# Optimization experiments

Hardware: AMD Instinct MI355X
Metric: run time of the kernel (lower is better)

Reference implementation:

```python
import jax, jax.numpy as jnp
import numpy as np

EMBED_DIM = 4096
NUM_Q_HEADS = 32
NUM_KV_HEADS = 8
HEAD_DIM = EMBED_DIM // NUM_Q_HEADS  # 128
GROUP = NUM_Q_HEADS // NUM_KV_HEADS  # 4
KV_SEQ_LEN = 1024
BATCH = 2
SEQ = 1024
THETA = 10000.0


def _rope(x, positions):
    # x: (B, T, H, D) with interleaved real/imag pairs along D (torch view_as_complex layout)
    half = x.shape[-1] // 2
    inv_freq = 1.0 / (THETA ** (jnp.arange(half, dtype=jnp.float32) / half))
    ang = positions[:, None].astype(jnp.float32) * inv_freq[None, :]  # (T, half)
    cos = jnp.cos(ang)[None, :, None, :].astype(x.dtype)
    sin = jnp.sin(ang)[None, :, None, :].astype(x.dtype)
    xr = x.reshape(*x.shape[:-1], half, 2)
    x0, x1 = xr[..., 0], xr[..., 1]
    o0 = x0 * cos - x1 * sin
    o1 = x0 * sin + x1 * cos
    return jnp.stack([o0, o1], axis=-1).reshape(x.shape)


def setup_inputs() -> dict:
    key = jax.random.key(0)
    ks = jax.random.split(key, 5)
    s_in = 1.0 / np.sqrt(EMBED_DIM)
    return {
        "x": jax.random.normal(ks[0], (BATCH, SEQ, EMBED_DIM), dtype=jnp.float32),
        "Wq": jax.random.normal(ks[1], (EMBED_DIM, EMBED_DIM), dtype=jnp.float32) * s_in,
        "Wk": jax.random.normal(ks[2], (NUM_KV_HEADS * HEAD_DIM, EMBED_DIM), dtype=jnp.float32) * s_in,
        "Wv": jax.random.normal(ks[3], (NUM_KV_HEADS * HEAD_DIM, EMBED_DIM), dtype=jnp.float32) * s_in,
        "Wo": jax.random.normal(ks[4], (EMBED_DIM, EMBED_DIM), dtype=jnp.float32) * s_in,
        "cache_k": jnp.zeros((BATCH, 2 * KV_SEQ_LEN, NUM_KV_HEADS, HEAD_DIM), dtype=jnp.float32),
        "cache_v": jnp.zeros((BATCH, 2 * KV_SEQ_LEN, NUM_KV_HEADS, HEAD_DIM), dtype=jnp.float32),
        "start_pos": 0,
    }


def reference(x, Wq, Wk, Wv, Wo, cache_k, cache_v, start_pos):
    B, T, C = x.shape
    end_pos = start_pos + T
    scale = 1.0 / np.sqrt(HEAD_DIM)

    q = (x @ Wq.T).reshape(B, T, NUM_Q_HEADS, HEAD_DIM)
    k = (x @ Wk.T).reshape(B, T, NUM_KV_HEADS, HEAD_DIM)
    v = (x @ Wv.T).reshape(B, T, NUM_KV_HEADS, HEAD_DIM)

    pos = start_pos + jnp.arange(T)
    q = _rope(q, pos)
    k = _rope(k, pos)

    # KV cache append (writes are detached in the original)
    cache_k = cache_k.at[:, start_pos:end_pos].set(jax.lax.stop_gradient(k))
    cache_v = cache_v.at[:, start_pos:end_pos].set(jax.lax.stop_gradient(v))
    k_full = cache_k[:, :end_pos]  # (B, S, Hkv, D)
    v_full = cache_v[:, :end_pos]

    # GQA without materializing repeated KV heads:
    # q head h attends kv head h // GROUP (matches repeat_interleave layout)
    q5 = q.transpose(0, 2, 1, 3).reshape(B, NUM_KV_HEADS, GROUP, T, HEAD_DIM)
    kh = k_full.transpose(0, 2, 1, 3)  # (B, Hkv, S, D)
    vh = v_full.transpose(0, 2, 1, 3)

    scores = jnp.einsum('bhgtd,bhsd->bhgts', q5, kh) * scale  # (B,Hkv,G,T,S)
    visible = jnp.arange(end_pos)[None, :] <= (start_pos + jnp.arange(T))[:, None]  # (T,S)
    scores = jnp.where(visible[None, None, None], scores, jnp.finfo(scores.dtype).min)
    probs = jax.nn.softmax(scores, axis=-1)
    ctx = jnp.einsum('bhgts,bhsd->bhgtd', probs, vh)

    out = ctx.reshape(B, NUM_Q_HEADS, T, HEAD_DIM).transpose(0, 2, 1, 3).reshape(B, T, C)
    return out @ Wo.T
```

## Files before the change

kernel.cpp:

```cpp
#include <hip/hip_runtime.h>
#include <stdint.h>

typedef unsigned short u16;
typedef __attribute__((ext_vector_type(8))) short short8x;
typedef __attribute__((ext_vector_type(4))) float floatx4;

#define TOKENS 2048
#define EMBED  4096
#define QKVN   6144
#define T_SEQ  1024
#define SMAX   2048
#define NQH    32
#define NKVH   8
#define HD     128

static __device__ __forceinline__ u16 f2b(float f) {
    union { float f; uint32_t u; } v; v.f = f;
    uint32_t r = v.u + 0x7fffu + ((v.u >> 16) & 1u);
    return (u16)(r >> 16);
}
static __device__ __forceinline__ float b2f(u16 h) {
    union { uint32_t u; float f; } v; v.u = ((uint32_t)h) << 16; return v.f;
}

static __device__ __forceinline__ void gload_lds16(const u16* g, u16* l) {
    __builtin_amdgcn_global_load_lds(
        (const __attribute__((address_space(1))) uint32_t*)g,
        (__attribute__((address_space(3))) uint32_t*)l, 16, 0, 0);
}

#define CSEG0 2097152
#define CSEG1 6291456
#define CSEG2 7340032
#define CSEG3 8388608
#define CSEG4 12582912
__global__ void convert_all_kernel(const float* __restrict__ x,  const float* __restrict__ Wq,
                                   const float* __restrict__ Wk, const float* __restrict__ Wv,
                                   const float* __restrict__ Wo,
                                   u16* __restrict__ xb, u16* __restrict__ wqkv,
                                   u16* __restrict__ wob) {
    int i = blockIdx.x * blockDim.x + threadIdx.x;
    if (i >= CSEG4) return;
    const float4* src; uint2* dst; int off;
    if (i < CSEG0)      { src = (const float4*)x;  dst = (uint2*)xb;   off = i; }
    else if (i < CSEG1) { src = (const float4*)Wq; dst = (uint2*)wqkv; off = i - CSEG0; }
    else if (i < CSEG2) { src = (const float4*)Wk; dst = (uint2*)wqkv + 4194304; off = i - CSEG1; }
    else if (i < CSEG3) { src = (const float4*)Wv; dst = (uint2*)wqkv + 5242880; off = i - CSEG2; }
    else                { src = (const float4*)Wo; dst = (uint2*)wob;  off = i - CSEG3; }
    float4 f = src[off];
    union { u16 h[4]; uint2 v; } o;
    o.h[0] = f2b(f.x); o.h[1] = f2b(f.y); o.h[2] = f2b(f.z); o.h[3] = f2b(f.w);
    dst[off] = o.v;
}

#define FENCE asm volatile("" ::: "memory")
#define WAITZ asm volatile("s_waitcnt vmcnt(0)" ::: "memory")
#define NOSTG ((void)0)
#define NOW   ((void)0)

#define HBA(BUF, H) (lds + (BUF) * 28672 + (H) * 8192)
#define HBB(BUF)    (lds + (BUF) * 28672 + 16384)
#define STGA(BUF, H, KT) do { \
    gload_lds16(gA[H][0] + (size_t)(KT) * 64, HBA(BUF, H) + dOffW); \
    gload_lds16(gA[H][1] + (size_t)(KT) * 64, HBA(BUF, H) + 4096 + dOffW); \
} while (0)
#define STGB(BUF, KT) do { \
    _Pragma("unroll") \
    for (int _L = 0; _L < 3; _L++) \
        gload_lds16(gBv[_L] + (size_t)(KT) * 64, HBB(BUF) + _L * 4096 + dOffW); \
} while (0)
#define STGALL(BUF, KT) do { STGA(BUF, 0, KT); STGA(BUF, 1, KT); STGB(BUF, KT); } while (0)
#define PH1(CBUF, STAGES, ENDW) do { \
    const u16* _pa0 = HBA(CBUF, 0); \
    const u16* _pa1 = HBA(CBUF, 1); \
    const u16* _pb  = HBB(CBUF); \
    short8x af0[4][2], af1[4][2], bf[3][2]; \
    _Pragma("unroll") \
    for (int _mi = 0; _mi < 4; _mi++) { \
        af0[_mi][0] = *(const short8x*)(_pa0 + offA[_mi][0]); \
        af0[_mi][1] = *(const short8x*)(_pa0 + offA[_mi][1]); } \
    _Pragma("unroll") \
    for (int _nj = 0; _nj < 3; _nj++) { \
        bf[_nj][0] = *(const short8x*)(_pb + offB[_nj][0]); \
        bf[_nj][1] = *(const short8x*)(_pb + offB[_nj][1]); } \
    STAGES; \
    __builtin_amdgcn_sched_barrier(0); \
    _Pragma("unroll") \
    for (int _mi = 0; _mi < 4; _mi++) { \
        af1[_mi][0] = *(const short8x*)(_pa1 + offA[_mi][0]); \
        af1[_mi][1] = *(const short8x*)(_pa1 + offA[_mi][1]); } \
    __builtin_amdgcn_s_setprio(1); \
    _Pragma("unroll") \
    for (int _kk = 0; _kk < 2; _kk++) \
        _Pragma("unroll") \
        for (int _mi = 0; _mi < 4; _mi++) \
            _Pragma("unroll") \
            for (int _nj = 0; _nj < 3; _nj++) \
                acc[0][_mi][_nj] = __builtin_amdgcn_mfma_f32_16x16x32_bf16( \
                    af0[_mi][_kk], bf[_nj][_kk], acc[0][_mi][_nj], 0, 0, 0); \
    _Pragma("unroll") \
    for (int _kk = 0; _kk < 2; _kk++) \
        _Pragma("unroll") \
        for (int _mi = 0; _mi < 4; _mi++) \
            _Pragma("unroll") \
            for (int _nj = 0; _nj < 3; _nj++) \
                acc[1][_mi][_nj] = __builtin_amdgcn_mfma_f32_16x16x32_bf16( \
                    af1[_mi][_kk], bf[_nj][_kk], acc[1][_mi][_nj], 0, 0, 0); \
    __builtin_amdgcn_s_setprio(0); \
    ENDW; \
    FENCE; __builtin_amdgcn_s_barrier(); FENCE; \
} while (0)

__global__ __launch_bounds__(512, 1) void gemm256_kernel(
    const u16* __restrict__ A, const u16* __restrict__ Bw,
    u16* __restrict__ Cv, int N, int K) {
    extern __shared__ __align__(16) u16 lds[];
    const int tid = threadIdx.x;
    const int lane = tid & 63, w = tid >> 6;
    const int quad = lane >> 4, lc = lane & 15;
    const int wm = w >> 2, wn = w & 3;
    const int Mbase = blockIdx.y * 256, Nbase = blockIdx.x * 192;

    const int r8 = lane >> 3;
    const int sl = (lane & 7) ^ r8;
    const int srow = w * 8 + r8;
    const u16* gA[2][2];
    const u16* gBv[3];
#pragma unroll
    for (int H = 0; H < 2; H++)
#pragma unroll
        for (int L = 0; L < 2; L++)
            gA[H][L] = A + (size_t)(Mbase + H * 128 + L * 64 + srow) * K + sl * 8;
#pragma unroll
    for (int L = 0; L < 3; L++)
        gBv[L] = Bw + (size_t)(Nbase + L * 64 + srow) * K + sl * 8;
    const int dOffW = w * 512;

    int offA[4][2], offB[3][2];
    const int xsw = lc & 7;
#pragma unroll
    for (int mi = 0; mi < 4; mi++)
#pragma unroll
        for (int kk = 0; kk < 2; kk++)
            offA[mi][kk] = (wm * 64 + mi * 16 + lc) * 64 + (((kk * 4 + quad) ^ xsw) * 8);
#pragma unroll
    for (int nj = 0; nj < 3; nj++)
#pragma unroll
        for (int kk = 0; kk < 2; kk++)
            offB[nj][kk] = (wn * 48 + nj * 16 + lc) * 64 + (((kk * 4 + quad) ^ xsw) * 8);

    floatx4 acc[2][4][3] = {};

    STGALL(0, 0);
    WAITZ;
    FENCE; __builtin_amdgcn_s_barrier(); FENCE;

    const int NT = K >> 6;
    for (int t = 0; t < NT - 2; t += 2) {
        PH1(0, STGALL(1, t + 1), WAITZ);
        PH1(1, STGALL(0, t + 2), WAITZ);
    }
    PH1(0, STGALL(1, NT - 1), WAITZ);
    PH1(1, NOSTG, NOW);

#pragma unroll
    for (int AH = 0; AH < 2; AH++)
#pragma unroll
        for (int mi = 0; mi < 4; mi++) {
            const int row0 = Mbase + AH * 128 + wm * 64 + mi * 16 + quad * 4;
#pragma unroll
            for (int nj = 0; nj < 3; nj++) {
                const int col = Nbase + wn * 48 + nj * 16 + lc;
#pragma unroll
                for (int r = 0; r < 4; r++)
                    Cv[(size_t)(row0 + r) * N + col] = f2b(acc[AH][mi][nj][r]);
            }
        }
}
#undef HBA
#undef HBB
#undef STGA
#undef STGB
#undef STGALL
#undef PH1

#define HA2(BUF, H) (lds + (BUF) * 24576 + (H) * 4096)
#define HBB2(BUF)   (lds + (BUF) * 24576 + 8192)
#define STGA2(BUF, H, KT) gload_lds16(gA2[H] + (size_t)(KT) * 64, HA2(BUF, H) + dOffW)
#define STGB2(BUF, KT) do { \
    _Pragma("unroll") \
    for (int _L = 0; _L < 4; _L++) \
        gload_lds16(gB2[_L] + (size_t)(KT) * 64, HBB2(BUF) + _L * 4096 + dOffW); \
} while (0)
#define STGALL2(BUF, KT) do { STGA2(BUF, 0, KT); STGA2(BUF, 1, KT); STGB2(BUF, KT); } while (0)
#define PH2(CBUF, STAGES, ENDW) do { \
    const u16* _pa0 = HA2(CBUF, 0); \
    const u16* _pa1 = HA2(CBUF, 1); \
    const u16* _pb  = HBB2(CBUF); \
    short8x af0[2][2], af1[2][2], bf2[4][2]; \
    _Pragma("unroll") \
    for (int _mi = 0; _mi < 2; _mi++) { \
        af0[_mi][0] = *(const short8x*)(_pa0 + offA2[_mi][0]); \
        af0[_mi][1] = *(const short8x*)(_pa0 + offA2[_mi][1]); } \
    _Pragma("unroll") \
    for (int _nj = 0; _nj < 4; _nj++) { \
        bf2[_nj][0] = *(const short8x*)(_pb + offB2[_nj][0]); \
        bf2[_nj][1] = *(const short8x*)(_pb + offB2[_nj][1]); } \
    STAGES; \
    __builtin_amdgcn_sched_barrier(0); \
    _Pragma("unroll") \
    for (int _mi = 0; _mi < 2; _mi++) { \
        af1[_mi][0] = *(const short8x*)(_pa1 + offA2[_mi][0]); \
        af1[_mi][1] = *(const short8x*)(_pa1 + offA2[_mi][1]); } \
    __builtin_amdgcn_s_setprio(1); \
    _Pragma("unroll") \
    for (int _kk = 0; _kk < 2; _kk++) \
        _Pragma("unroll") \
        for (int _mi = 0; _mi < 2; _mi++) \
            _Pragma("unroll") \
            for (int _nj = 0; _nj < 4; _nj++) \
                acc2[0][_mi][_nj] = __builtin_amdgcn_mfma_f32_16x16x32_bf16( \
                    af0[_mi][_kk], bf2[_nj][_kk], acc2[0][_mi][_nj], 0, 0, 0); \
    _Pragma("unroll") \
    for (int _kk = 0; _kk < 2; _kk++) \
        _Pragma("unroll") \
        for (int _mi = 0; _mi < 2; _mi++) \
            _Pragma("unroll") \
            for (int _nj = 0; _nj < 4; _nj++) \
                acc2[1][_mi][_nj] = __builtin_amdgcn_mfma_f32_16x16x32_bf16( \
                    af1[_mi][_kk], bf2[_nj][_kk], acc2[1][_mi][_nj], 0, 0, 0); \
    __builtin_amdgcn_s_setprio(0); \
    ENDW; \
    FENCE; __builtin_amdgcn_s_barrier(); FENCE; \
} while (0)

__global__ __launch_bounds__(512, 1) void gemmko_kernel(
    const u16* __restrict__ A, const u16* __restrict__ Bw,
    float* __restrict__ C, int N, int K) {
    extern __shared__ __align__(16) u16 lds[];
    const int tid = threadIdx.x;
    const int lane = tid & 63, w = tid >> 6;
    const int quad = lane >> 4, lc = lane & 15;
    const int wm = (w >> 2) & 1, wn = w & 3;
    const int Mbase = blockIdx.y * 128, Nbase = blockIdx.x * 256;

    const int r8 = lane >> 3;
    const int sl = (lane & 7) ^ r8;
    const int srow = w * 8 + r8;
    const u16* gA2[2];
    const u16* gB2[4];
#pragma unroll
    for (int H = 0; H < 2; H++)
        gA2[H] = A + (size_t)(Mbase + H * 64 + srow) * K + sl * 8;
#pragma unroll
    for (int L = 0; L < 4; L++)
        gB2[L] = Bw + (size_t)(Nbase + L * 64 + srow) * K + sl * 8;
    const int dOffW = w * 512;

    int offA2[2][2], offB2[4][2];
    const int xsw = lc & 7;
#pragma unroll
    for (int mi = 0; mi < 2; mi++)
#pragma unroll
        for (int kk = 0; kk < 2; kk++)
            offA2[mi][kk] = (wm * 32 + mi * 16 + lc) * 64 + (((kk * 4 + quad) ^ xsw) * 8);
#pragma unroll
    for (int nj = 0; nj < 4; nj++)
#pragma unroll
        for (int kk = 0; kk < 2; kk++)
            offB2[nj][kk] = (wn * 64 + nj * 16 + lc) * 64 + (((kk * 4 + quad) ^ xsw) * 8);

    floatx4 acc2[2][2][4] = {};

    STGALL2(0, 0);
    WAITZ;
    FENCE; __builtin_amdgcn_s_barrier(); FENCE;

    const int NT = K >> 6;
    for (int t = 0; t < NT - 2; t += 2) {
        PH2(0, STGALL2(1, t + 1), WAITZ);
        PH2(1, STGALL2(0, t + 2), WAITZ);
    }
    PH2(0, STGALL2(1, NT - 1), WAITZ);
    PH2(1, NOSTG, NOW);

#pragma unroll
    for (int AH = 0; AH < 2; AH++)
#pragma unroll
        for (int mi = 0; mi < 2; mi++) {
            const int row0 = Mbase + AH * 64 + wm * 32 + mi * 16 + quad * 4;
#pragma unroll
            for (int nj = 0; nj < 4; nj++) {
                const int col = Nbase + wn * 64 + nj * 16 + lc;
#pragma unroll
                for (int r = 0; r < 4; r++)
                    C[(size_t)(row0 + r) * N + col] = acc2[AH][mi][nj][r];
            }
        }
}
#undef HA2
#undef HBB2
#undef STGA2
#undef STGB2
#undef STGALL2
#undef PH2
#undef WAITZ
#undef NOSTG
#undef NOW
#undef FENCE

__global__ void cache_prefix_kernel(const float* __restrict__ ck, const float* __restrict__ cv,
                                    const int* __restrict__ sp,
                                    u16* __restrict__ kh, u16* __restrict__ vt8) {
    int spos = sp[0];
    long total = (long)2 * spos * NKVH * HD;
    for (long i = (long)blockIdx.x * blockDim.x + threadIdx.x; i < total; i += (long)gridDim.x * blockDim.x) {
        long d = i % HD, rest = i / HD;
        long g = rest % NKVH; rest /= NKVH;
        long s = rest % spos; long b = rest / spos;
        float kv = ck[((b * SMAX + s) * NKVH + g) * HD + d];
        kh[((b * NKVH + g) * SMAX + s) * HD + d] = f2b(kv);
        float vv = cv[((b * SMAX + s) * NKVH + g) * HD + d];
        vt8[(size_t)(b * NKVH + g) * SMAX * HD + (s >> 3) * 1024 + d * 8 + (s & 7)] = f2b(vv);
    }
}

__global__ void rope_qk_kernel(const u16* __restrict__ qkvb, const int* __restrict__ sp,
                               u16* __restrict__ qh, u16* __restrict__ kh) {
    int spos = sp[0];
    int idx = blockIdx.x * blockDim.x + threadIdx.x;
    int tok = idx / 2560;
    int u = idx - tok * 2560;
    int b = tok >> 10, t = tok & 1023;
    float pos = (float)(spos + t);
    const u16* src = qkvb + (size_t)tok * QKVN;
    const float kScale = 0.08838834764831845f;
    const float kLog = -0.20762050593045857f;
    if (u < 2048) {
        int h = u >> 6, i = u & 63;
        float ang = pos * exp2f((float)i * kLog);
        float cs = cosf(ang), sn = sinf(ang);
        float x0 = b2f(src[h * HD + 2 * i]), x1 = b2f(src[h * HD + 2 * i + 1]);
        size_t dst = (((size_t)(b * NQH + h) * T_SEQ) + t) * HD + 2 * i;
        qh[dst]     = f2b((x0 * cs - x1 * sn) * kScale);
        qh[dst + 1] = f2b((x0 * sn + x1 * cs) * kScale);
    } else {
        int u2 = u - 2048;
        int g = u2 >> 6, i = u2 & 63;
        float ang = pos * exp2f((float)i * kLog);
        float cs = cosf(ang), sn = sinf(ang);
        float x0 = b2f(src[EMBED + g * HD + 2 * i]), x1 = b2f(src[EMBED + g * HD + 2 * i + 1]);
        size_t dst = (((size_t)(b * NKVH + g) * SMAX) + spos + t) * HD + 2 * i;
        kh[dst]     = f2b(x0 * cs - x1 * sn);
        kh[dst + 1] = f2b(x0 * sn + x1 * cs);
    }
}

__global__ __launch_bounds__(256) void vpack_kernel(const u16* __restrict__ qkvb,
                                                    const int* __restrict__ sp,
                                                    u16* __restrict__ vt8) {
    __shared__ u16 lds[16 * 136];
    int spos = sp[0];
    int tile = blockIdx.x;
    int t16 = tile & 63;
    int g = (tile >> 6) & 7;
    int b = tile >> 9;
    int tok0 = t16 * 16;
    int tid = threadIdx.x;
    {
        int srow = tid >> 4, dc8 = (tid & 15) * 8;
        const u16* src = qkvb + (size_t)(b * T_SEQ + tok0 + srow) * QKVN + 5120 + g * HD + dc8;
        *(uint4*)(lds + srow * 136 + dc8) = *(const uint4*)src;
    }
    __syncthreads();
    int d = tid & 127, half = tid >> 7;
    u16* vpg = vt8 + (size_t)(b * NKVH + g) * SMAX * HD;
    int s0 = spos + tok0;
    u16 val[8];
#pragma unroll
    for (int k = 0; k < 8; k++) val[k] = lds[(half * 8 + k) * 136 + d];
    if ((s0 & 7) == 0) {
        union { u16 h[8]; uint4 u; } pk;
#pragma unroll
        for (int k = 0; k < 8; k++) pk.h[k] = val[k];
        *(uint4*)(vpg + (size_t)((s0 >> 3) + half) * 1024 + d * 8) = pk.u;
    } else {
#pragma unroll
        for (int k = 0; k < 8; k++) {
            int s = s0 + half * 8 + k;
            vpg[(size_t)(s >> 3) * 1024 + d * 8 + (s & 7)] = val[k];
        }
    }
}

__global__ __launch_bounds__(256, 2) void attn_kernel(
    const u16* __restrict__ qh, const u16* __restrict__ kh,
    const u16* __restrict__ vt8, const int* __restrict__ sp,
    u16* __restrict__ ctx) {
    extern __shared__ __align__(16) char smem[];
    int spos = sp[0];
    int tid = threadIdx.x, w = tid >> 6, lane = tid & 63;
    int quad = lane >> 4, lc = lane & 15;
    int tile = blockIdx.x;
    int j = 63 - (tile & 63);
    int g = (tile >> 6) & 7;
    int b = tile >> 9;
    int qbase = j * 16;

    const u16* kp = kh + (size_t)(b * NKVH + g) * SMAX * HD;
    const u16* vp = vt8 + (size_t)(b * NKVH + g) * SMAX * HD;

    short8x qf[4][4];
#pragma unroll
    for (int m = 0; m < 4; m++) {
        const u16* qp = qh + ((size_t)(b * NQH + g * 4 + m) * T_SEQ + qbase + lc) * HD + quad * 8;
#pragma unroll
        for (int dc = 0; dc < 4; dc++)
            qf[m][dc] = *(const short8x*)(qp + dc * 32);
    }
    short8x ones;
#pragma unroll
    for (int jj = 0; jj < 8; jj++) ones[jj] = (short)0x3F80;

    floatx4 o[4][8] = {};
    floatx4 lacc[4] = {};
    int rowpos = spos + qbase + quad * 4;
    int nch = (spos + qbase + 16 + 63) >> 6;
    u16* pw = (u16*)smem + w * 4608;

    for (int c = w; c < nch; c += 4) {
        int koff = c * 64;
#pragma unroll
        for (int st = 0; st < 4; st++) {
            const u16* kr = kp + (size_t)(koff + st * 16 + lc) * HD + quad * 8;
            floatx4 sc[4] = {};
#pragma unroll
            for (int dc = 0; dc < 4; dc++) {
                short8x kf = *(const short8x*)(kr + dc * 32);
#pragma unroll
                for (int m = 0; m < 4; m++)
                    sc[m] = __builtin_amdgcn_mfma_f32_16x16x32_bf16(qf[m][dc], kf, sc[m], 0, 0, 0);
            }
            int skey = koff + st * 16 + lc;
#pragma unroll
            for (int m = 0; m < 4; m++)
#pragma unroll
                for (int r = 0; r < 4; r++) {
                    float p = (skey <= rowpos + r) ? __expf(sc[m][r]) : 0.0f;
                    pw[m * 1152 + (quad * 4 + r) * 72 + st * 16 + lc] = f2b(p);
                }
        }
        asm volatile("s_waitcnt lgkmcnt(0)" ::: "memory");
#pragma unroll
        for (int hf = 0; hf < 2; hf++) {
            short8x pf[4];
#pragma unroll
            for (int m = 0; m < 4; m++)
                pf[m] = *(const short8x*)(pw + m * 1152 + lc * 72 + hf * 32 + quad * 8);
#pragma unroll
            for (int m = 0; m < 4; m++)
                lacc[m] = __builtin_amdgcn_mfma_f32_16x16x32_bf16(pf[m], ones, lacc[m], 0, 0, 0);
            const u16* vbase = vp + ((size_t)koff << 7) + (size_t)(hf * 4 + quad) * 1024 + lc * 8;
#pragma unroll
            for (int dc8 = 0; dc8 < 8; dc8++) {
                short8x vf = *(const short8x*)(vbase + dc8 * 128);
#pragma unroll
                for (int m = 0; m < 4; m++)
                    o[m][dc8] = __builtin_amdgcn_mfma_f32_16x16x32_bf16(pf[m], vf, o[m][dc8], 0, 0, 0);
            }
        }
    }

    float* obuf = (float*)smem;
    float* lbuf = (float*)(smem + 33792);
    for (int ph = 0; ph < 4; ph++) {
        __syncthreads();
        if (w == ph) {
            if (ph == 0) {
#pragma unroll
                for (int m = 0; m < 4; m++) {
#pragma unroll
                    for (int dc8 = 0; dc8 < 8; dc8++)
#pragma unroll
                        for (int r = 0; r < 4; r++)
                            obuf[(m * 16 + quad * 4 + r) * 132 + dc8 * 16 + lc] = o[m][dc8][r];
#pragma unroll
                    for (int r = 0; r < 4; r++) lbuf[m * 16 + quad * 4 + r] = lacc[m][r];
                }
            } else {
#pragma unroll
                for (int m = 0; m < 4; m++) {
#pragma unroll
                    for (int dc8 = 0; dc8 < 8; dc8++)
#pragma unroll
                        for (int r = 0; r < 4; r++)
                            obuf[(m * 16 + quad * 4 + r) * 132 + dc8 * 16 + lc] += o[m][dc8][r];
#pragma unroll
                    for (int r = 0; r < 4; r++) lbuf[m * 16 + quad * 4 + r] += lacc[m][r];
                }
            }
        }
    }
    __syncthreads();

    int row = tid >> 2;
    int m = row >> 4;
    int cb = (tid & 3) * 32;
    float inv = 1.0f / lbuf[row];
    int token = qbase + (row & 15);
    size_t base = ((size_t)(b * T_SEQ + token) * NQH + g * 4 + m) * HD + cb;
#pragma unroll
    for (int v4 = 0; v4 < 4; v4++) {
        union { u16 h[8]; uint4 u; } pk;
#pragma unroll
        for (int jj = 0; jj < 8; jj++)
            pk.h[jj] = f2b(obuf[row * 132 + cb + v4 * 8 + jj] * inv);
        *(uint4*)(ctx + base + v4 * 8) = pk.u;
    }
}

extern "C" void kernel_launch(void* const* d_in, const int* in_sizes, int n_in,
                              void* d_out, int out_size, void* d_ws, size_t ws_size,
                              hipStream_t stream) {
    const float* x  = (const float*)d_in[0];
    const float* Wq = (const float*)d_in[1];
    const float* Wk = (const float*)d_in[2];
    const float* Wv = (const float*)d_in[3];
    const float* Wo = (const float*)d_in[4];
    const float* ck = (const float*)d_in[5];
    const float* cv = (const float*)d_in[6];
    const int*   sp = (const int*)d_in[7];

    char* p = (char*)d_ws;
    u16* xb   = (u16*)p;
    u16* qh   = xb;
    p += (size_t)TOKENS * EMBED * 2;
    u16* wqkv = (u16*)p; p += (size_t)QKVN * EMBED * 2;
    u16* wob  = (u16*)p; p += (size_t)EMBED * EMBED * 2;
    u16* qkvb = (u16*)p;
    u16* ctx  = qkvb;
    p += (size_t)TOKENS * QKVN * 2;
    u16* kh   = (u16*)p; p += (size_t)2 * NKVH * SMAX * HD * 2;
    u16* vt8  = (u16*)p;

    static int gemm_attr = 0;
    if (!gemm_attr) {
        (void)hipFuncSetAttribute(reinterpret_cast<const void*>(&gemm256_kernel),
                                  hipFuncAttributeMaxDynamicSharedMemorySize, 114688);
        (void)hipFuncSetAttribute(reinterpret_cast<const void*>(&gemmko_kernel),
                                  hipFuncAttributeMaxDynamicSharedMemorySize, 98304);
        gemm_attr = 1;
    }

    convert_all_kernel<<<(CSEG4 + 255) / 256, 256, 0, stream>>>(x, Wq, Wk, Wv, Wo, xb, wqkv, wob);
    gemm256_kernel<<<dim3(QKVN / 192, TOKENS / 256), 512, 114688, stream>>>(xb, wqkv, qkvb, QKVN, EMBED);
    cache_prefix_kernel<<<256, 256, 0, stream>>>(ck, cv, sp, kh, vt8);
    rope_qk_kernel<<<TOKENS * 2560 / 256, 256, 0, stream>>>(qkvb, sp, qh, kh);
    vpack_kernel<<<1024, 256, 0, stream>>>(qkvb, sp, vt8);
    attn_kernel<<<1024, 256, 36864, stream>>>(qh, kh, vt8, sp, ctx);
    gemmko_kernel<<<dim3(EMBED / 256, TOKENS / 128), 512, 98304, stream>>>(ctx, wob, (float*)d_out, EMBED, EMBED);
}
```

Measured before the change: 314.8 us.

## Retile QKV GEMM to 128x192 blocks with 4 waves and K-step 32

The QKV projection GEMM moves from 256x192 tiles with 8 waves and a 64-wide K step to 128x192 tiles with 4 waves, a 32-wide K step, and 40 KB of LDS. Each wave now computes a 64x96 sub-tile with a 4x6 MFMA block. The swizzle and staging are redone for 32-element rows, and the launch bound becomes (256,2) so two blocks can share a CU. The aim is more blocks (512 vs 256) and better occupancy and latency hiding on 256 CUs. The cost is less reuse per block and twice as many barriers per unit of K.

After: 328.7 us. +4.4%, slower.

```diff
diff --git a/kernel.cpp b/kernel.cpp
--- a/kernel.cpp
+++ b/kernel.cpp
@@ -58,131 +58,95 @@
 #define NOSTG ((void)0)
 #define NOW   ((void)0)
 
-#define HBA(BUF, H) (lds + (BUF) * 28672 + (H) * 8192)
-#define HBB(BUF)    (lds + (BUF) * 28672 + 16384)
-#define STGA(BUF, H, KT) do { \
-    gload_lds16(gA[H][0] + (size_t)(KT) * 64, HBA(BUF, H) + dOffW); \
-    gload_lds16(gA[H][1] + (size_t)(KT) * 64, HBA(BUF, H) + 4096 + dOffW); \
+#define STG1(BUF, KT) do { \
+    _Pragma("unroll") \
+    for (int _i = 0; _i < 5; _i++) \
+        gload_lds16(gsrc[_i] + (size_t)(KT) * 32, lds + (BUF) * 10240 + ldst[_i]); \
 } while (0)
-#define STGB(BUF, KT) do { \
-    _Pragma("unroll") \
-    for (int _L = 0; _L < 3; _L++) \
-        gload_lds16(gBv[_L] + (size_t)(KT) * 64, HBB(BUF) + _L * 4096 + dOffW); \
-} while (0)
-#define STGALL(BUF, KT) do { STGA(BUF, 0, KT); STGA(BUF, 1, KT); STGB(BUF, KT); } while (0)
-#define PH1(CBUF, STAGES, ENDW) do { \
-    const u16* _pa0 = HBA(CBUF, 0); \
-    const u16* _pa1 = HBA(CBUF, 1); \
-    const u16* _pb  = HBB(CBUF); \
-    short8x af0[4][2], af1[4][2], bf[3][2]; \
-    _Pragma("unroll") \
-    for (int _mi = 0; _mi < 4; _mi++) { \
-        af0[_mi][0] = *(const short8x*)(_pa0 + offA[_mi][0]); \
-        af0[_mi][1] = *(const short8x*)(_pa0 + offA[_mi][1]); } \
-    _Pragma("unroll") \
-    for (int _nj = 0; _nj < 3; _nj++) { \
-        bf[_nj][0] = *(const short8x*)(_pb + offB[_nj][0]); \
-        bf[_nj][1] = *(const short8x*)(_pb + offB[_nj][1]); } \
+#define PH(CBUF, STAGES, ENDW) do { \
+    const u16* _p = lds + (CBUF) * 10240; \
+    short8x af[4], bf[6]; \
+    _Pragma("unroll") \
+    for (int _mi = 0; _mi < 4; _mi++) af[_mi] = *(const short8x*)(_p + offA[_mi]); \
+    _Pragma("unroll") \
+    for (int _nj = 0; _nj < 6; _nj++) bf[_nj] = *(const short8x*)(_p + offB[_nj]); \
     STAGES; \
     __builtin_amdgcn_sched_barrier(0); \
-    _Pragma("unroll") \
-    for (int _mi = 0; _mi < 4; _mi++) { \
-        af1[_mi][0] = *(const short8x*)(_pa1 + offA[_mi][0]); \
-        af1[_mi][1] = *(const short8x*)(_pa1 + offA[_mi][1]); } \
     __builtin_amdgcn_s_setprio(1); \
     _Pragma("unroll") \
-    for (int _kk = 0; _kk < 2; _kk++) \
+    for (int _mi = 0; _mi < 4; _mi++) \
         _Pragma("unroll") \
-        for (int _mi = 0; _mi < 4; _mi++) \
-            _Pragma("unroll") \
-            for (int _nj = 0; _nj < 3; _nj++) \
-                acc[0][_mi][_nj] = __builtin_amdgcn_mfma_f32_16x16x32_bf16( \
-                    af0[_mi][_kk], bf[_nj][_kk], acc[0][_mi][_nj], 0, 0, 0); \
-    _Pragma("unroll") \
-    for (int _kk = 0; _kk < 2; _kk++) \
-        _Pragma("unroll") \
-        for (int _mi = 0; _mi < 4; _mi++) \
-            _Pragma("unroll") \
-            for (int _nj = 0; _nj < 3; _nj++) \
-                acc[1][_mi][_nj] = __builtin_amdgcn_mfma_f32_16x16x32_bf16( \
-                    af1[_mi][_kk], bf[_nj][_kk], acc[1][_mi][_nj], 0, 0, 0); \
+        for (int _nj = 0; _nj < 6; _nj++) \
+            acc[_mi][_nj] = __builtin_amdgcn_mfma_f32_16x16x32_bf16( \
+                af[_mi], bf[_nj], acc[_mi][_nj], 0, 0, 0); \
     __builtin_amdgcn_s_setprio(0); \
     ENDW; \
     FENCE; __builtin_amdgcn_s_barrier(); FENCE; \
 } while (0)
 
-__global__ __launch_bounds__(512, 1) void gemm256_kernel(
+__global__ __launch_bounds__(256, 2) void gemm256_kernel(
     const u16* __restrict__ A, const u16* __restrict__ Bw,
     u16* __restrict__ Cv, int N, int K) {
     extern __shared__ __align__(16) u16 lds[];
     const int tid = threadIdx.x;
     const int lane = tid & 63, w = tid >> 6;
     const int quad = lane >> 4, lc = lane & 15;
-    const int wm = w >> 2, wn = w & 3;
-    const int Mbase = blockIdx.y * 256, Nbase = blockIdx.x * 192;
-
-    const int r8 = lane >> 3;
-    const int sl = (lane & 7) ^ r8;
-    const int srow = w * 8 + r8;
-    const u16* gA[2][2];
-    const u16* gBv[3];
-#pragma unroll
-    for (int H = 0; H < 2; H++)
-#pragma unroll
-        for (int L = 0; L < 2; L++)
-            gA[H][L] = A + (size_t)(Mbase + H * 128 + L * 64 + srow) * K + sl * 8;
-#pragma unroll
-    for (int L = 0; L < 3; L++)
-        gBv[L] = Bw + (size_t)(Nbase + L * 64 + srow) * K + sl * 8;
-    const int dOffW = w * 512;
-
-    int offA[4][2], offB[3][2];
-    const int xsw = lc & 7;
-#pragma unroll
-    for (int mi = 0; mi < 4; mi++)
-#pragma unroll
-        for (int kk = 0; kk < 2; kk++)
-            offA[mi][kk] = (wm * 64 + mi * 16 + lc) * 64 + (((kk * 4 + quad) ^ xsw) * 8);
-#pragma unroll
-    for (int nj = 0; nj < 3; nj++)
-#pragma unroll
-        for (int kk = 0; kk < 2; kk++)
-            offB[nj][kk] = (wn * 48 + nj * 16 + lc) * 64 + (((kk * 4 + quad) ^ xsw) * 8);
-
-    floatx4 acc[2][4][3] = {};
-
-    STGALL(0, 0);
+    const int wm = w >> 1, wn = w & 1;
+    const int Mbase = blockIdx.y * 128, Nbase = blockIdx.x * 192;
+
+    const int r16 = lane >> 2;
+    const int q   = (lane & 3) ^ ((lane >> 3) & 3);
+    const u16* gsrc[5];
+    int ldst[5];
+#pragma unroll
+    for (int i = 0; i < 5; i++) {
+        int c = w + i * 4;
+        if (c < 8) gsrc[i] = A  + (size_t)(Mbase + c * 16 + r16) * K + q * 8;
+        else       gsrc[i] = Bw + (size_t)(Nbase + (c - 8) * 16 + r16) * K + q * 8;
+        ldst[i] = c * 512;
+    }
+
+    int offA[4], offB[6];
+    const int xsw = (lc >> 1) & 3;
+#pragma unroll
+    for (int mi = 0; mi < 4; mi++) {
+        int row = wm * 64 + mi * 16 + lc;
+        offA[mi] = row * 32 + ((quad ^ xsw) * 8);
+    }
+#pragma unroll
+    for (int nj = 0; nj < 6; nj++) {
+        int row = wn * 96 + nj * 16 + lc;
+        offB[nj] = 4096 + row * 32 + ((quad ^ xsw) * 8);
+    }
+
+    floatx4 acc[4][6] = {};
+
+    STG1(0, 0);
     WAITZ;
     FENCE; __builtin_amdgcn_s_barrier(); FENCE;
 
-    const int NT = K >> 6;
+    const int NT = K >> 5;
     for (int t = 0; t < NT - 2; t += 2) {
-        PH1(0, STGALL(1, t + 1), WAITZ);
-        PH1(1, STGALL(0, t + 2), WAITZ);
-    }
-    PH1(0, STGALL(1, NT - 1), WAITZ);
-    PH1(1, NOSTG, NOW);
-
-#pragma unroll
-    for (int AH = 0; AH < 2; AH++)
-#pragma unroll
-        for (int mi = 0; mi < 4; mi++) {
-            const int row0 = Mbase + AH * 128 + wm * 64 + mi * 16 + quad * 4;
-#pragma unroll
-            for (int nj = 0; nj < 3; nj++) {
-                const int col = Nbase + wn * 48 + nj * 16 + lc;
-#pragma unroll
-                for (int r = 0; r < 4; r++)
-                    Cv[(size_t)(row0 + r) * N + col] = f2b(acc[AH][mi][nj][r]);
-            }
+        PH(0, STG1(1, t + 1), WAITZ);
+        PH(1, STG1(0, t + 2), WAITZ);
+    }
+    PH(0, STG1(1, NT - 1), WAITZ);
+    PH(1, NOSTG, NOW);
+
+#pragma unroll
+    for (int mi = 0; mi < 4; mi++) {
+        const int row0 = Mbase + wm * 64 + mi * 16 + quad * 4;
+#pragma unroll
+        for (int nj = 0; nj < 6; nj++) {
+            const int col = Nbase + wn * 96 + nj * 16 + lc;
+#pragma unroll
+            for (int r = 0; r < 4; r++)
+                Cv[(size_t)(row0 + r) * N + col] = f2b(acc[mi][nj][r]);
         }
-}
-#undef HBA
-#undef HBB
-#undef STGA
-#undef STGB
-#undef STGALL
-#undef PH1
+    }
+}
+#undef STG1
+#undef PH
 
 #define HA2(BUF, H) (lds + (BUF) * 24576 + (H) * 4096)
 #define HBB2(BUF)   (lds + (BUF) * 24576 + 8192)
@@ -546,14 +510,14 @@
     static int gemm_attr = 0;
     if (!gemm_attr) {
         (void)hipFuncSetAttribute(reinterpret_cast<const void*>(&gemm256_kernel),
-                                  hipFuncAttributeMaxDynamicSharedMemorySize, 114688);
+                                  hipFuncAttributeMaxDynamicSharedMemorySize, 40960);
         (void)hipFuncSetAttribute(reinterpret_cast<const void*>(&gemmko_kernel),
                                   hipFuncAttributeMaxDynamicSharedMemorySize, 98304);
         gemm_attr = 1;
     }
 
     convert_all_kernel<<<(CSEG4 + 255) / 256, 256, 0, stream>>>(x, Wq, Wk, Wv, Wo, xb, wqkv, wob);
-    gemm256_kernel<<<dim3(QKVN / 192, TOKENS / 256), 512, 114688, stream>>>(xb, wqkv, qkvb, QKVN, EMBED);
+    gemm256_kernel<<<dim3(QKVN / 192, TOKENS / 128), 256, 40960, stream>>>(xb, wqkv, qkvb, QKVN, EMBED);
     cache_prefix_kernel<<<256, 256, 0, stream>>>(ck, cv, sp, kh, vt8);
     rope_qk_kernel<<<TOKENS * 2560 / 256, 256, 0, stream>>>(qkvb, sp, qh, kh);
     vpack_kernel<<<1024, 256, 0, stream>>>(qkvb, sp, vt8);
```

## Assign one query head per wave in attention instead of splitting keys across waves

Applied to the files above, without the earlier changes.

Each of the four waves now processes a single query head of the GQA group over all key chunks, rather than every wave handling all four heads over a strided subset of key chunks. This removes the cross-wave reduction through shared memory and its barriers, shrinks per-wave accumulator registers, and allows launch bounds of four blocks per CU with a small static LDS buffer. In exchange, each wave now loads every K/V chunk itself, so K/V global traffic per block is roughly four times higher and fragments are no longer shared across heads. The final output is written as scattered 2-byte stores instead of packed 16-byte stores.

Result: slower. 363.6 us (+15.5%).

```diff
diff --git a/kernel.cpp b/kernel.cpp
--- a/kernel.cpp
+++ b/kernel.cpp
@@ -393,11 +393,11 @@
     }
 }
 
-__global__ __launch_bounds__(256, 2) void attn_kernel(
+__global__ __launch_bounds__(256, 4) void attn_kernel(
     const u16* __restrict__ qh, const u16* __restrict__ kh,
     const u16* __restrict__ vt8, const int* __restrict__ sp,
     u16* __restrict__ ctx) {
-    extern __shared__ __align__(16) char smem[];
+    __shared__ u16 pws[4][1152];
     int spos = sp[0];
     int tid = threadIdx.x, w = tid >> 6, lane = tid & 63;
     int quad = lane >> 4, lc = lane & 15;
@@ -406,116 +406,68 @@
     int g = (tile >> 6) & 7;
     int b = tile >> 9;
     int qbase = j * 16;
+    int m = w;
 
     const u16* kp = kh + (size_t)(b * NKVH + g) * SMAX * HD;
     const u16* vp = vt8 + (size_t)(b * NKVH + g) * SMAX * HD;
 
-    short8x qf[4][4];
-#pragma unroll
-    for (int m = 0; m < 4; m++) {
+    short8x qf[4];
+    {
         const u16* qp = qh + ((size_t)(b * NQH + g * 4 + m) * T_SEQ + qbase + lc) * HD + quad * 8;
 #pragma unroll
         for (int dc = 0; dc < 4; dc++)
-            qf[m][dc] = *(const short8x*)(qp + dc * 32);
+            qf[dc] = *(const short8x*)(qp + dc * 32);
     }
     short8x ones;
 #pragma unroll
     for (int jj = 0; jj < 8; jj++) ones[jj] = (short)0x3F80;
 
-    floatx4 o[4][8] = {};
-    floatx4 lacc[4] = {};
+    floatx4 o[8] = {};
+    floatx4 lacc = {};
     int rowpos = spos + qbase + quad * 4;
     int nch = (spos + qbase + 16 + 63) >> 6;
-    u16* pw = (u16*)smem + w * 4608;
-
-    for (int c = w; c < nch; c += 4) {
+    u16* pw = pws[w];
+
+    for (int c = 0; c < nch; c++) {
         int koff = c * 64;
 #pragma unroll
         for (int st = 0; st < 4; st++) {
             const u16* kr = kp + (size_t)(koff + st * 16 + lc) * HD + quad * 8;
-            floatx4 sc[4] = {};
+            floatx4 sc = {};
 #pragma unroll
             for (int dc = 0; dc < 4; dc++) {
                 short8x kf = *(const short8x*)(kr + dc * 32);
-#pragma unroll
-                for (int m = 0; m < 4; m++)
-                    sc[m] = __builtin_amdgcn_mfma_f32_16x16x32_bf16(qf[m][dc], kf, sc[m], 0, 0, 0);
+                sc = __builtin_amdgcn_mfma_f32_16x16x32_bf16(qf[dc], kf, sc, 0, 0, 0);
             }
             int skey = koff + st * 16 + lc;
 #pragma unroll
-            for (int m = 0; m < 4; m++)
-#pragma unroll
-                for (int r = 0; r < 4; r++) {
-                    float p = (skey <= rowpos + r) ? __expf(sc[m][r]) : 0.0f;
-                    pw[m * 1152 + (quad * 4 + r) * 72 + st * 16 + lc] = f2b(p);
-                }
+            for (int r = 0; r < 4; r++) {
+                float p = (skey <= rowpos + r) ? __expf(sc[r]) : 0.0f;
+                pw[(quad * 4 + r) * 72 + st * 16 + lc] = f2b(p);
+            }
         }
         asm volatile("s_waitcnt lgkmcnt(0)" ::: "memory");
 #pragma unroll
         for (int hf = 0; hf < 2; hf++) {
-            short8x pf[4];
-#pragma unroll
-            for (int m = 0; m < 4; m++)
-                pf[m] = *(const short8x*)(pw + m * 1152 + lc * 72 + hf * 32 + quad * 8);
-#pragma unroll
-            for (int m = 0; m < 4; m++)
-                lacc[m] = __builtin_amdgcn_mfma_f32_16x16x32_bf16(pf[m], ones, lacc[m], 0, 0, 0);
+            short8x pf = *(const short8x*)(pw + lc * 72 + hf * 32 + quad * 8);
+            lacc = __builtin_amdgcn_mfma_f32_16x16x32_bf16(pf, ones, lacc, 0, 0, 0);
             const u16* vbase = vp + ((size_t)koff << 7) + (size_t)(hf * 4 + quad) * 1024 + lc * 8;
 #pragma unroll
             for (int dc8 = 0; dc8 < 8; dc8++) {
                 short8x vf = *(const short8x*)(vbase + dc8 * 128);
-#pragma unroll
-                for (int m = 0; m < 4; m++)
-                    o[m][dc8] = __builtin_amdgcn_mfma_f32_16x16x32_bf16(pf[m], vf, o[m][dc8], 0, 0, 0);
+                o[dc8] = __builtin_amdgcn_mfma_f32_16x16x32_bf16(pf, vf, o[dc8], 0, 0, 0);
             }
         }
     }
 
-    float* obuf = (float*)smem;
-    float* lbuf = (float*)(smem + 33792);
-    for (int ph = 0; ph < 4; ph++) {
-        __syncthreads();
-        if (w == ph) {
-            if (ph == 0) {
-#pragma unroll
-                for (int m = 0; m < 4; m++) {
-#pragma unroll
-                    for (int dc8 = 0; dc8 < 8; dc8++)
-#pragma unroll
-                        for (int r = 0; r < 4; r++)
-                            obuf[(m * 16 + quad * 4 + r) * 132 + dc8 * 16 + lc] = o[m][dc8][r];
-#pragma unroll
-                    for (int r = 0; r < 4; r++) lbuf[m * 16 + quad * 4 + r] = lacc[m][r];
-                }
-            } else {
-#pragma unroll
-                for (int m = 0; m < 4; m++) {
-#pragma unroll
-                    for (int dc8 = 0; dc8 < 8; dc8++)
-#pragma unroll
-                        for (int r = 0; r < 4; r++)
-                            obuf[(m * 16 + quad * 4 + r) * 132 + dc8 * 16 + lc] += o[m][dc8][r];
-#pragma unroll
-                    for (int r = 0; r < 4; r++) lbuf[m * 16 + quad * 4 + r] += lacc[m][r];
-                }
-            }
-        }
-    }
-    __syncthreads();
-
-    int row = tid >> 2;
-    int m = row >> 4;
-    int cb = (tid & 3) * 32;
-    float inv = 1.0f / lbuf[row];
-    int token = qbase + (row & 15);
-    size_t base = ((size_t)(b * T_SEQ + token) * NQH + g * 4 + m) * HD + cb;
-#pragma unroll
-    for (int v4 = 0; v4 < 4; v4++) {
-        union { u16 h[8]; uint4 u; } pk;
-#pragma unroll
-        for (int jj = 0; jj < 8; jj++)
-            pk.h[jj] = f2b(obuf[row * 132 + cb + v4 * 8 + jj] * inv);
-        *(uint4*)(ctx + base + v4 * 8) = pk.u;
+#pragma unroll
+    for (int r = 0; r < 4; r++) {
+        float inv = 1.0f / lacc[r];
+        int token = qbase + quad * 4 + r;
+        size_t base = ((size_t)(b * T_SEQ + token) * NQH + g * 4 + m) * HD + lc;
+#pragma unroll
+        for (int dc8 = 0; dc8 < 8; dc8++)
+            ctx[base + dc8 * 16] = f2b(o[dc8][r] * inv);
     }
 }
 
@@ -557,6 +509,6 @@
     cache_prefix_kernel<<<256, 256, 0, stream>>>(ck, cv, sp, kh, vt8);
     rope_qk_kernel<<<TOKENS * 2560 / 256, 256, 0, stream>>>(qkvb, sp, qh, kh);
     vpack_kernel<<<1024, 256, 0, stream>>>(qkvb, sp, vt8);
-    attn_kernel<<<1024, 256, 36864, stream>>>(qh, kh, vt8, sp, ctx);
+    attn_kernel<<<1024, 256, 0, stream>>>(qh, kh, vt8, sp, ctx);
     gemmko_kernel<<<dim3(EMBED / 256, TOKENS / 128), 512, 98304, stream>>>(ctx, wob, (float*)d_out, EMBED, EMBED);
 }
```
